# Performance work log

Measured on AMD Instinct MI355X. Metric: run time of the kernel, lower is better.

Reference implementation:

```python
import jax, jax.numpy as jnp
import numpy as np

B, T, DIM, H = 2, 2048, 512, 8
EPS = 1e-6


def setup_inputs() -> dict:
    key = jax.random.key(0)
    ks = jax.random.split(key, 6)
    scale = 0.05  # keep activations in a sane range for softmax/elu
    return {
        "x": jax.random.normal(ks[0], (B, T, DIM), dtype=jnp.float32),
        "Wq": jax.random.normal(ks[1], (DIM, DIM), dtype=jnp.float32) * scale,
        "Wk": jax.random.normal(ks[2], (DIM, DIM), dtype=jnp.float32) * scale,
        "Wv": jax.random.normal(ks[3], (DIM, DIM), dtype=jnp.float32) * scale,
        "Wo": jax.random.normal(ks[4], (DIM, DIM), dtype=jnp.float32) * scale,
        "bo": jax.random.normal(ks[5], (DIM,), dtype=jnp.float32) * scale,
    }


def reference(x, Wq, Wk, Wv, Wo, bo):
    b, t, dim = x.shape
    h = H
    d = dim // h
    # projections (nn.Linear: x @ W.T)
    q = x @ Wq.T
    k = x @ Wk.T
    v = x @ Wv.T
    mh = lambda z: z.reshape(b, t, h, d).transpose(0, 2, 1, 3)  # [b,h,t,d]
    q, k, v = mh(q), mh(k), mh(v)
    # causal linear attention with buckets = n (bucket size 1, no shift)
    q = jax.nn.softmax(q, axis=-1)
    k = jax.nn.elu(k) + 1.0  # psi
    k_cumsum = jnp.cumsum(k, axis=2)                       # [b,h,t,d]
    context = jnp.einsum('bhnd,bhne->bhnde', k, v)         # per-position outer products
    context = jnp.cumsum(context, axis=2)                  # causal prefix sum, [b,h,t,d,d]
    context = context / (k_cumsum[..., None] + EPS)        # safe_div
    attn = jnp.einsum('bhnd,bhnde->bhne', q, context)      # [b,h,t,d]
    out = attn.transpose(0, 2, 1, 3).reshape(b, t, dim)
    return out @ Wo.T + bo
```

## Files before the change

kernel.cpp:

```cpp
#include <hip/hip_runtime.h>

#define T_SEQ 2048
#define DIMM 512
#define NH 8
#define HD 64
#define BB 2
#define CHUNK 64
#define NCHUNK 32
#define EPSV 1e-6f
#define LDST 72
#define CST 66

typedef __attribute__((ext_vector_type(8))) short bf16x8;
typedef __attribute__((ext_vector_type(4))) short s16x4;
typedef __attribute__((ext_vector_type(4))) float f32x4;

static __device__ inline short f2bf(float f) {
    union { float f; unsigned u; } v; v.f = f;
    unsigned r = v.u + 0x7FFFu + ((v.u >> 16) & 1u);
    return (short)(r >> 16);
}
static __device__ inline float bf2f(short s) {
    union { unsigned u; float f; } v; v.u = ((unsigned)(unsigned short)s) << 16;
    return v.f;
}
static __device__ __forceinline__ void gload_lds16(const void* g, void* l) {
    __builtin_amdgcn_global_load_lds(
        (__attribute__((address_space(1))) void*)g,
        (__attribute__((address_space(3))) void*)l, 16, 0, 0);
}

__global__ __launch_bounds__(256) void convert_kernel(
    const float* __restrict__ x, const float* __restrict__ Wq,
    const float* __restrict__ Wk, const float* __restrict__ Wv,
    const float* __restrict__ Wo,
    short* __restrict__ xb, short* __restrict__ Wcat, short* __restrict__ Wob)
{
    const int u = blockIdx.x * 256 + threadIdx.x;
    const float* src; short* dst;
    if (u < 262144) {
        src = x + (size_t)u * 8; dst = xb + (size_t)u * 8;
    } else {
        const int v = u - 262144;
        const int o = (v & 32767) * 8;
        if (v < 32768)       { src = Wq + o; dst = Wcat + o; }
        else if (v < 65536)  { src = Wk + o; dst = Wcat + 262144 + o; }
        else if (v < 98304)  { src = Wv + o; dst = Wcat + 524288 + o; }
        else                 { src = Wo + o; dst = Wob + o; }
    }
    const float4 a = *(const float4*)src;
    const float4 b = *(const float4*)(src + 4);
    *(bf16x8*)dst = (bf16x8){f2bf(a.x), f2bf(a.y), f2bf(a.z), f2bf(a.w),
                             f2bf(b.x), f2bf(b.y), f2bf(b.z), f2bf(b.w)};
}

__global__ __launch_bounds__(256) void proj_mfma_kernel(
    const short* __restrict__ xb, const short* __restrict__ Wcat,
    short* __restrict__ Qs, short* __restrict__ Kbf,
    short* __restrict__ Ktb, short* __restrict__ Vt)
{
    __shared__ short S[8192];
    short* As = S;
    short* Bs = S + 4096;
    short* Cs = S;
    const int nblk = blockIdx.x;
    const int m0 = blockIdx.y * 64;
    const int n0 = nblk * 64;
    const int which = nblk >> 3;
    const int head = nblk & 7;
    const int tid = threadIdx.x;
    const int lane = tid & 63, w = tid >> 6;
    const int fr = lane & 15, fg = lane >> 4;
    const int lr = lane >> 3, lc = (lane & 7) * 8;
    f32x4 acc[4] = {};
    for (int k0 = 0; k0 < DIMM; k0 += 64) {
        #pragma unroll
        for (int it = 0; it < 2; it++) {
            const int r0 = w * 16 + it * 8;
            gload_lds16(xb + (size_t)(m0 + r0 + lr) * DIMM + k0 + lc, &As[r0 * 64]);
            gload_lds16(Wcat + (size_t)(n0 + r0 + lr) * DIMM + k0 + lc, &Bs[r0 * 64]);
        }
        __syncthreads();
        #pragma unroll
        for (int ks = 0; ks < 2; ks++) {
            const bf16x8 af = *(const bf16x8*)&As[(w * 16 + fr) * 64 + ks * 32 + fg * 8];
            #pragma unroll
            for (int j = 0; j < 4; j++) {
                const bf16x8 bfr = *(const bf16x8*)&Bs[(j * 16 + fr) * 64 + ks * 32 + fg * 8];
                acc[j] = __builtin_amdgcn_mfma_f32_16x16x32_bf16(af, bfr, acc[j], 0, 0, 0);
            }
        }
        __syncthreads();
    }
    #pragma unroll
    for (int j = 0; j < 4; j++)
        #pragma unroll
        for (int reg = 0; reg < 4; reg++) {
            float val = acc[j][reg];
            if (which == 1) val = (val > 0.f) ? (val + 1.f) : __expf(val);
            Cs[(w * 16 + fg * 4 + reg) * CST + j * 16 + fr] = f2bf(val);
        }
    __syncthreads();

    const int b = m0 >> 11, t0 = m0 & (T_SEQ - 1);
    if (which == 0) {
        if (tid < 64) {
            const unsigned* cr = (const unsigned*)&Cs[tid * CST];
            unsigned u[32];
            #pragma unroll
            for (int s = 0; s < 32; s++) u[s] = cr[s];
            float mx = -1e30f;
            #pragma unroll
            for (int s = 0; s < 32; s++) {
                mx = fmaxf(mx, bf2f((short)(u[s] & 0xffff)));
                mx = fmaxf(mx, bf2f((short)(u[s] >> 16)));
            }
            float sum = 0.f;
            #pragma unroll
            for (int s = 0; s < 32; s++) {
                sum += __expf(bf2f((short)(u[s] & 0xffff)) - mx);
                sum += __expf(bf2f((short)(u[s] >> 16)) - mx);
            }
            const float inv = 1.f / sum;
            short* qp = Qs + (((size_t)(b * NH + head)) * T_SEQ + t0 + tid) * HD;
            #pragma unroll
            for (int g = 0; g < 8; g++) {
                bf16x8 o;
                #pragma unroll
                for (int k = 0; k < 4; k++) {
                    const unsigned uv = u[g * 4 + k];
                    o[2 * k]     = f2bf(__expf(bf2f((short)(uv & 0xffff)) - mx) * inv);
                    o[2 * k + 1] = f2bf(__expf(bf2f((short)(uv >> 16)) - mx) * inv);
                }
                *(bf16x8*)(qp + g * 8) = o;
            }
        }
    } else if (which == 1) {
        if (tid < 64) {
            const unsigned* cr = (const unsigned*)&Cs[tid * CST];
            short* kp = Kbf + (((size_t)(b * NH + head)) * T_SEQ + t0 + tid) * HD;
            #pragma unroll
            for (int g = 0; g < 8; g++) {
                bf16x8 o;
                #pragma unroll
                for (int k = 0; k < 4; k++) {
                    const unsigned uv = cr[g * 4 + k];
                    o[2 * k]     = (short)(uv & 0xffff);
                    o[2 * k + 1] = (short)(uv >> 16);
                }
                *(bf16x8*)(kp + g * 8) = o;
            }
        }
        {
            const int c = tid & 63, q = tid >> 6;
            short* ktp = Ktb + (((size_t)(b * NH + head)) * HD + c) * T_SEQ + t0 + q * 16;
            #pragma unroll
            for (int s = 0; s < 2; s++) {
                bf16x8 o;
                #pragma unroll
                for (int k = 0; k < 8; k++) o[k] = Cs[(q * 16 + s * 8 + k) * CST + c];
                *(bf16x8*)(ktp + s * 8) = o;
            }
        }
    } else {
        const int c = tid & 63, q = tid >> 6;
        short* vtp = Vt + (((size_t)(b * NH + head)) * HD + c) * T_SEQ + t0 + q * 16;
        #pragma unroll
        for (int s = 0; s < 2; s++) {
            bf16x8 o;
            #pragma unroll
            for (int k = 0; k < 8; k++) o[k] = Cs[(q * 16 + s * 8 + k) * CST + c];
            *(bf16x8*)(vtp + s * 8) = o;
        }
    }
}

__global__ __launch_bounds__(256) void chunk_sum_kernel(
    const short* __restrict__ Ktb, const short* __restrict__ Vt,
    float* __restrict__ Schunk, float* __restrict__ kchunk)
{
    __shared__ short VtL[64 * LDST];
    __shared__ short KtL[64 * LDST];
    __shared__ float ksp[4][64];
    const int bh = blockIdx.x >> 5, c = blockIdx.x & 31;
    const int tid = threadIdx.x;
    const int lane = tid & 63, w = tid >> 6;
    const int fr = lane & 15, fg = lane >> 4;
    #pragma unroll
    for (int it = 0; it < 2; it++) {
        const int qi = it * 256 + tid;
        const int r = qi >> 3, c8 = (qi & 7) * 8;
        *(bf16x8*)&VtL[r * LDST + c8] =
            *(const bf16x8*)(Vt + ((size_t)(bh * HD) + r) * T_SEQ + c * CHUNK + c8);
        *(bf16x8*)&KtL[r * LDST + c8] =
            *(const bf16x8*)(Ktb + ((size_t)(bh * HD) + r) * T_SEQ + c * CHUNK + c8);
    }
    __syncthreads();
    f32x4 acc[4] = {};
    #pragma unroll
    for (int ks = 0; ks < 2; ks++) {
        const bf16x8 av = *(const bf16x8*)&VtL[(w * 16 + fr) * LDST + ks * 32 + fg * 8];
        #pragma unroll
        for (int j = 0; j < 4; j++) {
            const bf16x8 bk = *(const bf16x8*)&KtL[(j * 16 + fr) * LDST + ks * 32 + fg * 8];
            acc[j] = __builtin_amdgcn_mfma_f32_16x16x32_bf16(av, bk, acc[j], 0, 0, 0);
        }
    }
    float* Sout = Schunk + ((size_t)bh * NCHUNK + c) * 4096;
    #pragma unroll
    for (int j = 0; j < 4; j++)
        #pragma unroll
        for (int reg = 0; reg < 4; reg++)
            Sout[(w * 16 + fg * 4 + reg) * 64 + j * 16 + fr] = acc[j][reg];
    float ps = 0.f;
    #pragma unroll
    for (int t = 0; t < 16; t++) ps += bf2f(KtL[lane * LDST + w * 16 + t]);
    ksp[w][lane] = ps;
    __syncthreads();
    if (tid < 64)
        kchunk[((size_t)bh * NCHUNK + c) * 64 + tid] =
            ksp[0][tid] + ksp[1][tid] + ksp[2][tid] + ksp[3][tid];
}

__global__ __launch_bounds__(256) void scan_kernel(float* __restrict__ Schunk,
                                                   float* __restrict__ kchunk)
{
    const int gid = blockIdx.x * 256 + threadIdx.x;
    if (blockIdx.x < 256) {
        const int bh = gid >> 12, i = gid & 4095;
        float run = 0.f;
        float* p = Schunk + (size_t)bh * NCHUNK * 4096 + i;
        for (int c = 0; c < NCHUNK; c++) { const float tv = p[c * 4096]; p[c * 4096] = run; run += tv; }
    } else {
        const int idx = gid - 65536;
        const int bh = idx >> 6, d = idx & 63;
        float run = 0.f;
        float* p = kchunk + (size_t)bh * NCHUNK * 64 + d;
        for (int c = 0; c < NCHUNK; c++) { const float tv = p[c * 64]; p[c * 64] = run; run += tv; }
    }
}

__global__ __launch_bounds__(256) void intra_kernel(
    const short* __restrict__ Qs, const short* __restrict__ Kbf,
    const short* __restrict__ Vt, const float* __restrict__ Schunk,
    const float* __restrict__ kchunk, short* __restrict__ attnb)
{
    __shared__ short B1[64 * LDST];
    __shared__ short B2[64 * LDST];
    __shared__ short KL[64 * LDST];
    __shared__ short VtL[64 * LDST];
    __shared__ short QnL[64 * LDST];
    __shared__ float gsum[4][64];
    __shared__ float kpre[64];
    const int bh = blockIdx.x >> 5, c = blockIdx.x & 31;
    const int tid = threadIdx.x;
    const int lane = tid & 63, w = tid >> 6;
    const int fr = lane & 15, fg = lane >> 4;
    const size_t tdbase = ((size_t)bh * T_SEQ + c * CHUNK) * HD;
    #pragma unroll
    for (int it = 0; it < 2; it++) {
        const int qi = it * 256 + tid;
        const int r = qi >> 3, c8 = (qi & 7) * 8;
        *(bf16x8*)&B1[r * LDST + c8]  = *(const bf16x8*)(Qs + tdbase + r * HD + c8);
        *(bf16x8*)&KL[r * LDST + c8]  = *(const bf16x8*)(Kbf + tdbase + r * HD + c8);
        *(bf16x8*)&VtL[r * LDST + c8] =
            *(const bf16x8*)(Vt + ((size_t)(bh * HD) + r) * T_SEQ + c * CHUNK + c8);
    }
    {
        const float* Sp = Schunk + ((size_t)bh * NCHUNK + c) * 4096;
        #pragma unroll
        for (int it = 0; it < 4; it++) {
            const int qi = it * 256 + tid;
            const int r = qi >> 4, c4 = (qi & 15) * 4;
            const float4 v = *(const float4*)(Sp + r * 64 + c4);
            *(s16x4*)&B2[r * LDST + c4] = (s16x4){f2bf(v.x), f2bf(v.y), f2bf(v.z), f2bf(v.w)};
        }
    }
    if (tid < 64) kpre[tid] = kchunk[((size_t)bh * NCHUNK + c) * 64 + tid];
    __syncthreads();
    {
        float s = 0.f;
        #pragma unroll
        for (int t = 0; t < 16; t++) s += bf2f(KL[(w * 16 + t) * LDST + lane]);
        gsum[w][lane] = s;
    }
    __syncthreads();
    {
        float run = kpre[lane];
        for (int gg = 0; gg < w; gg++) run += gsum[gg][lane];
        #pragma unroll
        for (int t0 = 0; t0 < 16; t0++) {
            const int t = w * 16 + t0;
            run += bf2f(KL[t * LDST + lane]);
            const float qv = bf2f(B1[t * LDST + lane]);
            QnL[t * LDST + lane] = f2bf(qv / (run + EPSV));
        }
    }
    __syncthreads();
    {
        f32x4 a1[4] = {};
        #pragma unroll
        for (int ks = 0; ks < 2; ks++) {
            const bf16x8 aq = *(const bf16x8*)&QnL[(w * 16 + fr) * LDST + ks * 32 + fg * 8];
            #pragma unroll
            for (int j = 0; j < 4; j++) {
                const bf16x8 bk = *(const bf16x8*)&KL[(j * 16 + fr) * LDST + ks * 32 + fg * 8];
                a1[j] = __builtin_amdgcn_mfma_f32_16x16x32_bf16(aq, bk, a1[j], 0, 0, 0);
            }
        }
        const int trow = w * 16 + fg * 4;
        #pragma unroll
        for (int j = 0; j < 4; j++)
            #pragma unroll
            for (int reg = 0; reg < 4; reg++) {
                const int t = trow + reg, s = j * 16 + fr;
                B1[t * LDST + s] = (s <= t) ? f2bf(a1[j][reg]) : (short)0;
            }
    }
    __syncthreads();
    {
        f32x4 a2[4] = {};
        #pragma unroll
        for (int ks = 0; ks < 2; ks++) {
            const bf16x8 aq = *(const bf16x8*)&QnL[(w * 16 + fr) * LDST + ks * 32 + fg * 8];
            const bf16x8 aa = *(const bf16x8*)&B1[(w * 16 + fr) * LDST + ks * 32 + fg * 8];
            #pragma unroll
            for (int j = 0; j < 4; j++) {
                const bf16x8 bs = *(const bf16x8*)&B2[(j * 16 + fr) * LDST + ks * 32 + fg * 8];
                const bf16x8 bv = *(const bf16x8*)&VtL[(j * 16 + fr) * LDST + ks * 32 + fg * 8];
                a2[j] = __builtin_amdgcn_mfma_f32_16x16x32_bf16(aq, bs, a2[j], 0, 0, 0);
                a2[j] = __builtin_amdgcn_mfma_f32_16x16x32_bf16(aa, bv, a2[j], 0, 0, 0);
            }
        }
        short* ap = attnb + tdbase;
        const int trow = w * 16 + fg * 4;
        #pragma unroll
        for (int j = 0; j < 4; j++)
            #pragma unroll
            for (int reg = 0; reg < 4; reg++)
                ap[(trow + reg) * HD + j * 16 + fr] = f2bf(a2[j][reg]);
    }
}

__global__ __launch_bounds__(256) void outproj_mfma_kernel(
    const short* __restrict__ attnb, const short* __restrict__ Wob,
    const float* __restrict__ bo, float* __restrict__ out)
{
    __shared__ short As[64 * 64];
    __shared__ short Bs[64 * 64];
    const int m0 = blockIdx.x * 64;
    const int n0 = blockIdx.y * 64;
    const int tid = threadIdx.x;
    const int lane = tid & 63, w = tid >> 6;
    const int fr = lane & 15, fg = lane >> 4;
    const int lr = lane >> 3, lc = (lane & 7) * 8;
    const int b = m0 >> 11, tbase = m0 & (T_SEQ - 1);
    f32x4 acc[4] = {};
    for (int k0 = 0; k0 < DIMM; k0 += 64) {
        const int h = k0 >> 6;
        #pragma unroll
        for (int it = 0; it < 2; it++) {
            const int r0 = w * 16 + it * 8;
            gload_lds16(attnb + (((size_t)(b * NH + h)) * T_SEQ + tbase + r0 + lr) * HD + lc,
                        &As[r0 * 64]);
            gload_lds16(Wob + (size_t)(n0 + r0 + lr) * DIMM + k0 + lc, &Bs[r0 * 64]);
        }
        __syncthreads();
        #pragma unroll
        for (int ks = 0; ks < 2; ks++) {
            const bf16x8 af = *(const bf16x8*)&As[(w * 16 + fr) * 64 + ks * 32 + fg * 8];
            #pragma unroll
            for (int j = 0; j < 4; j++) {
                const bf16x8 bfr = *(const bf16x8*)&Bs[(j * 16 + fr) * 64 + ks * 32 + fg * 8];
                acc[j] = __builtin_amdgcn_mfma_f32_16x16x32_bf16(af, bfr, acc[j], 0, 0, 0);
            }
        }
        __syncthreads();
    }
    #pragma unroll
    for (int j = 0; j < 4; j++)
        #pragma unroll
        for (int reg = 0; reg < 4; reg++) {
            const int m = m0 + w * 16 + fg * 4 + reg;
            const int n = n0 + j * 16 + fr;
            out[(size_t)m * DIMM + n] = acc[j][reg] + bo[n];
        }
}

extern "C" void kernel_launch(void* const* d_in, const int* in_sizes, int n_in,
                              void* d_out, int out_size, void* d_ws, size_t ws_size,
                              hipStream_t stream)
{
    const float* x  = (const float*)d_in[0];
    const float* Wq = (const float*)d_in[1];
    const float* Wk = (const float*)d_in[2];
    const float* Wv = (const float*)d_in[3];
    const float* Wo = (const float*)d_in[4];
    const float* bo = (const float*)d_in[5];
    float* out = (float*)d_out;

    const size_t NELEM = (size_t)BB * T_SEQ * DIMM;
    short* xb    = (short*)d_ws;
    short* Wcat  = xb + NELEM;
    short* Wob   = Wcat + 786432;
    short* Qs    = Wob + 262144;
    short* Kbf   = Qs + NELEM;
    short* Ktb   = Kbf + NELEM;
    short* Vt    = Ktb + NELEM;
    short* attnb = Vt + NELEM;
    float* Schunk = (float*)(attnb + NELEM);
    float* kchunk = Schunk + (size_t)BB * NH * NCHUNK * 4096;

    convert_kernel<<<dim3(1536), 256, 0, stream>>>(x, Wq, Wk, Wv, Wo, xb, Wcat, Wob);
    proj_mfma_kernel<<<dim3(24, 64), 256, 0, stream>>>(xb, Wcat, Qs, Kbf, Ktb, Vt);
    chunk_sum_kernel<<<dim3(BB * NH * NCHUNK), 256, 0, stream>>>(Ktb, Vt, Schunk, kchunk);
    scan_kernel<<<dim3(260), 256, 0, stream>>>(Schunk, kchunk);
    intra_kernel<<<dim3(BB * NH * NCHUNK), 256, 0, stream>>>(Qs, Kbf, Vt, Schunk, kchunk, attnb);
    outproj_mfma_kernel<<<dim3(64, 8), 256, 0, stream>>>(attnb, Wob, bo, out);
}
```

Baseline: 64.02 us.

## Fuse QKV projection per head with chunk state computation and swizzle LDS

The projection kernel now computes Q, K and V for one head and a 64-row tile in a single block of 12 MFMA accumulators, and reuses the shared x tile across all three. The chunk-sum kernel is folded in, so the per-chunk K^T V state and the K column sums are computed straight from the LDS tile instead of being re-read from global memory. An XOR swizzle is applied to the LDS tile layout to reduce bank conflicts. In exchange there are fewer blocks (512 instead of 1536), more registers per thread and a larger LDS footprint, and the fused epilogue does strided scalar LDS reads.

```diff
diff --git a/kernel.cpp b/kernel.cpp
--- a/kernel.cpp
+++ b/kernel.cpp
@@ -9,7 +9,7 @@
 #define NCHUNK 32
 #define EPSV 1e-6f
 #define LDST 72
-#define CST 66
+#define CST2 198
 
 typedef __attribute__((ext_vector_type(8))) short bf16x8;
 typedef __attribute__((ext_vector_type(4))) short s16x4;
@@ -54,172 +54,161 @@
                              f2bf(b.x), f2bf(b.y), f2bf(b.z), f2bf(b.w)};
 }
 
-__global__ __launch_bounds__(256) void proj_mfma_kernel(
+__global__ __launch_bounds__(256) void fusedproj_kernel(
     const short* __restrict__ xb, const short* __restrict__ Wcat,
     short* __restrict__ Qs, short* __restrict__ Kbf,
-    short* __restrict__ Ktb, short* __restrict__ Vt)
-{
-    __shared__ short S[8192];
+    short* __restrict__ Ktb, short* __restrict__ Vt,
+    float* __restrict__ Schunk, float* __restrict__ kchunk)
+{
+    __shared__ short S[16384];
     short* As = S;
     short* Bs = S + 4096;
     short* Cs = S;
-    const int nblk = blockIdx.x;
+    const int h = blockIdx.x;
     const int m0 = blockIdx.y * 64;
-    const int n0 = nblk * 64;
-    const int which = nblk >> 3;
-    const int head = nblk & 7;
+    const int b = m0 >> 11;
+    const int t0 = m0 & (T_SEQ - 1);
+    const int c = t0 >> 6;
+    const int bh = b * NH + h;
     const int tid = threadIdx.x;
     const int lane = tid & 63, w = tid >> 6;
     const int fr = lane & 15, fg = lane >> 4;
-    const int lr = lane >> 3, lc = (lane & 7) * 8;
-    f32x4 acc[4] = {};
+    const int lr = lane >> 3;
+    const int sl8 = ((lane & 7) ^ lr) * 8;
+    const int xr = fr & 7;
+    f32x4 acc[12] = {};
+
     for (int k0 = 0; k0 < DIMM; k0 += 64) {
         #pragma unroll
         for (int it = 0; it < 2; it++) {
             const int r0 = w * 16 + it * 8;
-            gload_lds16(xb + (size_t)(m0 + r0 + lr) * DIMM + k0 + lc, &As[r0 * 64]);
-            gload_lds16(Wcat + (size_t)(n0 + r0 + lr) * DIMM + k0 + lc, &Bs[r0 * 64]);
+            gload_lds16(xb + (size_t)(m0 + r0 + lr) * DIMM + k0 + sl8, &As[r0 * 64]);
+        }
+        #pragma unroll
+        for (int it = 0; it < 6; it++) {
+            const int rb0 = w * 48 + it * 8;
+            const int rb = rb0 + lr;
+            const int p = rb >> 6;
+            const int gr = p * DIMM + h * 64 + (rb & 63);
+            gload_lds16(Wcat + (size_t)gr * DIMM + k0 + sl8, &Bs[rb0 * 64]);
         }
         __syncthreads();
         #pragma unroll
         for (int ks = 0; ks < 2; ks++) {
-            const bf16x8 af = *(const bf16x8*)&As[(w * 16 + fr) * 64 + ks * 32 + fg * 8];
-            #pragma unroll
-            for (int j = 0; j < 4; j++) {
-                const bf16x8 bfr = *(const bf16x8*)&Bs[(j * 16 + fr) * 64 + ks * 32 + fg * 8];
-                acc[j] = __builtin_amdgcn_mfma_f32_16x16x32_bf16(af, bfr, acc[j], 0, 0, 0);
+            const int cc = (((ks << 2) + fg) ^ xr) * 8;
+            const bf16x8 af = *(const bf16x8*)&As[(w * 16 + fr) * 64 + cc];
+            #pragma unroll
+            for (int jj = 0; jj < 12; jj++) {
+                const bf16x8 bfr = *(const bf16x8*)&Bs[(jj * 16 + fr) * 64 + cc];
+                acc[jj] = __builtin_amdgcn_mfma_f32_16x16x32_bf16(af, bfr, acc[jj], 0, 0, 0);
             }
         }
         __syncthreads();
     }
+
     #pragma unroll
-    for (int j = 0; j < 4; j++)
+    for (int jj = 0; jj < 12; jj++)
         #pragma unroll
         for (int reg = 0; reg < 4; reg++) {
-            float val = acc[j][reg];
-            if (which == 1) val = (val > 0.f) ? (val + 1.f) : __expf(val);
-            Cs[(w * 16 + fg * 4 + reg) * CST + j * 16 + fr] = f2bf(val);
+            float val = acc[jj][reg];
+            if (jj >= 4 && jj < 8) val = (val > 0.f) ? (val + 1.f) : __expf(val);
+            Cs[(w * 16 + fg * 4 + reg) * CST2 + jj * 16 + fr] = f2bf(val);
         }
     __syncthreads();
 
-    const int b = m0 >> 11, t0 = m0 & (T_SEQ - 1);
-    if (which == 0) {
-        if (tid < 64) {
-            const unsigned* cr = (const unsigned*)&Cs[tid * CST];
-            unsigned u[32];
-            #pragma unroll
-            for (int s = 0; s < 32; s++) u[s] = cr[s];
-            float mx = -1e30f;
-            #pragma unroll
-            for (int s = 0; s < 32; s++) {
-                mx = fmaxf(mx, bf2f((short)(u[s] & 0xffff)));
-                mx = fmaxf(mx, bf2f((short)(u[s] >> 16)));
-            }
-            float sum = 0.f;
-            #pragma unroll
-            for (int s = 0; s < 32; s++) {
-                sum += __expf(bf2f((short)(u[s] & 0xffff)) - mx);
-                sum += __expf(bf2f((short)(u[s] >> 16)) - mx);
-            }
-            const float inv = 1.f / sum;
-            short* qp = Qs + (((size_t)(b * NH + head)) * T_SEQ + t0 + tid) * HD;
-            #pragma unroll
-            for (int g = 0; g < 8; g++) {
-                bf16x8 o;
+    if (tid < 64) {
+        const int r = tid;
+        const unsigned* cr = (const unsigned*)&Cs[r * CST2];
+        unsigned u[32];
+        #pragma unroll
+        for (int s = 0; s < 32; s++) u[s] = cr[s];
+        float mx = -1e30f;
+        #pragma unroll
+        for (int s = 0; s < 32; s++) {
+            mx = fmaxf(mx, bf2f((short)(u[s] & 0xffff)));
+            mx = fmaxf(mx, bf2f((short)(u[s] >> 16)));
+        }
+        float sum = 0.f;
+        #pragma unroll
+        for (int s = 0; s < 32; s++) {
+            sum += __expf(bf2f((short)(u[s] & 0xffff)) - mx);
+            sum += __expf(bf2f((short)(u[s] >> 16)) - mx);
+        }
+        const float inv = 1.f / sum;
+        short* qp = Qs + ((size_t)bh * T_SEQ + t0 + r) * HD;
+        #pragma unroll
+        for (int g = 0; g < 8; g++) {
+            bf16x8 o;
+            #pragma unroll
+            for (int k = 0; k < 4; k++) {
+                const unsigned uv = u[g * 4 + k];
+                o[2 * k]     = f2bf(__expf(bf2f((short)(uv & 0xffff)) - mx) * inv);
+                o[2 * k + 1] = f2bf(__expf(bf2f((short)(uv >> 16)) - mx) * inv);
+            }
+            *(bf16x8*)(qp + g * 8) = o;
+        }
+    } else if (tid < 128) {
+        const int r = tid - 64;
+        const unsigned* cr = (const unsigned*)&Cs[r * CST2 + 64];
+        short* kp = Kbf + ((size_t)bh * T_SEQ + t0 + r) * HD;
+        #pragma unroll
+        for (int g = 0; g < 8; g++) {
+            bf16x8 o;
+            #pragma unroll
+            for (int k = 0; k < 4; k++) {
+                const unsigned uv = cr[g * 4 + k];
+                o[2 * k]     = (short)(uv & 0xffff);
+                o[2 * k + 1] = (short)(uv >> 16);
+            }
+            *(bf16x8*)(kp + g * 8) = o;
+        }
+    }
+    {
+        const int col = tid & 63, q = tid >> 6;
+        short* ktp = Ktb + ((size_t)bh * HD + col) * T_SEQ + t0 + q * 16;
+        short* vtp = Vt  + ((size_t)bh * HD + col) * T_SEQ + t0 + q * 16;
+        #pragma unroll
+        for (int s = 0; s < 2; s++) {
+            bf16x8 ok, ov;
+            #pragma unroll
+            for (int k = 0; k < 8; k++) {
+                ok[k] = Cs[(q * 16 + s * 8 + k) * CST2 + 64 + col];
+                ov[k] = Cs[(q * 16 + s * 8 + k) * CST2 + 128 + col];
+            }
+            *(bf16x8*)(ktp + s * 8) = ok;
+            *(bf16x8*)(vtp + s * 8) = ov;
+        }
+    }
+    {
+        f32x4 a2[4] = {};
+        #pragma unroll
+        for (int ks = 0; ks < 2; ks++) {
+            bf16x8 av;
+            #pragma unroll
+            for (int uu = 0; uu < 8; uu++)
+                av[uu] = Cs[(ks * 32 + fg * 8 + uu) * CST2 + 128 + w * 16 + fr];
+            #pragma unroll
+            for (int jj = 0; jj < 4; jj++) {
+                bf16x8 bk;
                 #pragma unroll
-                for (int k = 0; k < 4; k++) {
-                    const unsigned uv = u[g * 4 + k];
-                    o[2 * k]     = f2bf(__expf(bf2f((short)(uv & 0xffff)) - mx) * inv);
-                    o[2 * k + 1] = f2bf(__expf(bf2f((short)(uv >> 16)) - mx) * inv);
-                }
-                *(bf16x8*)(qp + g * 8) = o;
-            }
-        }
-    } else if (which == 1) {
-        if (tid < 64) {
-            const unsigned* cr = (const unsigned*)&Cs[tid * CST];
-            short* kp = Kbf + (((size_t)(b * NH + head)) * T_SEQ + t0 + tid) * HD;
-            #pragma unroll
-            for (int g = 0; g < 8; g++) {
-                bf16x8 o;
-                #pragma unroll
-                for (int k = 0; k < 4; k++) {
-                    const unsigned uv = cr[g * 4 + k];
-                    o[2 * k]     = (short)(uv & 0xffff);
-                    o[2 * k + 1] = (short)(uv >> 16);
-                }
-                *(bf16x8*)(kp + g * 8) = o;
-            }
-        }
-        {
-            const int c = tid & 63, q = tid >> 6;
-            short* ktp = Ktb + (((size_t)(b * NH + head)) * HD + c) * T_SEQ + t0 + q * 16;
-            #pragma unroll
-            for (int s = 0; s < 2; s++) {
-                bf16x8 o;
-                #pragma unroll
-                for (int k = 0; k < 8; k++) o[k] = Cs[(q * 16 + s * 8 + k) * CST + c];
-                *(bf16x8*)(ktp + s * 8) = o;
-            }
-        }
-    } else {
-        const int c = tid & 63, q = tid >> 6;
-        short* vtp = Vt + (((size_t)(b * NH + head)) * HD + c) * T_SEQ + t0 + q * 16;
-        #pragma unroll
-        for (int s = 0; s < 2; s++) {
-            bf16x8 o;
-            #pragma unroll
-            for (int k = 0; k < 8; k++) o[k] = Cs[(q * 16 + s * 8 + k) * CST + c];
-            *(bf16x8*)(vtp + s * 8) = o;
-        }
-    }
-}
-
-__global__ __launch_bounds__(256) void chunk_sum_kernel(
-    const short* __restrict__ Ktb, const short* __restrict__ Vt,
-    float* __restrict__ Schunk, float* __restrict__ kchunk)
-{
-    __shared__ short VtL[64 * LDST];
-    __shared__ short KtL[64 * LDST];
-    __shared__ float ksp[4][64];
-    const int bh = blockIdx.x >> 5, c = blockIdx.x & 31;
-    const int tid = threadIdx.x;
-    const int lane = tid & 63, w = tid >> 6;
-    const int fr = lane & 15, fg = lane >> 4;
-    #pragma unroll
-    for (int it = 0; it < 2; it++) {
-        const int qi = it * 256 + tid;
-        const int r = qi >> 3, c8 = (qi & 7) * 8;
-        *(bf16x8*)&VtL[r * LDST + c8] =
-            *(const bf16x8*)(Vt + ((size_t)(bh * HD) + r) * T_SEQ + c * CHUNK + c8);
-        *(bf16x8*)&KtL[r * LDST + c8] =
-            *(const bf16x8*)(Ktb + ((size_t)(bh * HD) + r) * T_SEQ + c * CHUNK + c8);
-    }
-    __syncthreads();
-    f32x4 acc[4] = {};
-    #pragma unroll
-    for (int ks = 0; ks < 2; ks++) {
-        const bf16x8 av = *(const bf16x8*)&VtL[(w * 16 + fr) * LDST + ks * 32 + fg * 8];
-        #pragma unroll
-        for (int j = 0; j < 4; j++) {
-            const bf16x8 bk = *(const bf16x8*)&KtL[(j * 16 + fr) * LDST + ks * 32 + fg * 8];
-            acc[j] = __builtin_amdgcn_mfma_f32_16x16x32_bf16(av, bk, acc[j], 0, 0, 0);
-        }
-    }
-    float* Sout = Schunk + ((size_t)bh * NCHUNK + c) * 4096;
-    #pragma unroll
-    for (int j = 0; j < 4; j++)
-        #pragma unroll
-        for (int reg = 0; reg < 4; reg++)
-            Sout[(w * 16 + fg * 4 + reg) * 64 + j * 16 + fr] = acc[j][reg];
-    float ps = 0.f;
-    #pragma unroll
-    for (int t = 0; t < 16; t++) ps += bf2f(KtL[lane * LDST + w * 16 + t]);
-    ksp[w][lane] = ps;
-    __syncthreads();
-    if (tid < 64)
-        kchunk[((size_t)bh * NCHUNK + c) * 64 + tid] =
-            ksp[0][tid] + ksp[1][tid] + ksp[2][tid] + ksp[3][tid];
+                for (int uu = 0; uu < 8; uu++)
+                    bk[uu] = Cs[(ks * 32 + fg * 8 + uu) * CST2 + 64 + jj * 16 + fr];
+                a2[jj] = __builtin_amdgcn_mfma_f32_16x16x32_bf16(av, bk, a2[jj], 0, 0, 0);
+            }
+        }
+        float* Sout = Schunk + ((size_t)bh * NCHUNK + c) * 4096;
+        #pragma unroll
+        for (int jj = 0; jj < 4; jj++)
+            #pragma unroll
+            for (int reg = 0; reg < 4; reg++)
+                Sout[(w * 16 + fg * 4 + reg) * 64 + jj * 16 + fr] = a2[jj][reg];
+    }
+    if (tid < 64) {
+        float s = 0.f;
+        #pragma unroll
+        for (int t = 0; t < 64; t++) s += bf2f(Cs[t * CST2 + 64 + tid]);
+        kchunk[((size_t)bh * NCHUNK + c) * 64 + tid] = s;
+    }
 }
 
 __global__ __launch_bounds__(256) void scan_kernel(float* __restrict__ Schunk,
@@ -412,8 +401,8 @@
     float* kchunk = Schunk + (size_t)BB * NH * NCHUNK * 4096;
 
     convert_kernel<<<dim3(1536), 256, 0, stream>>>(x, Wq, Wk, Wv, Wo, xb, Wcat, Wob);
-    proj_mfma_kernel<<<dim3(24, 64), 256, 0, stream>>>(xb, Wcat, Qs, Kbf, Ktb, Vt);
-    chunk_sum_kernel<<<dim3(BB * NH * NCHUNK), 256, 0, stream>>>(Ktb, Vt, Schunk, kchunk);
+    fusedproj_kernel<<<dim3(8, 64), 256, 0, stream>>>(xb, Wcat, Qs, Kbf, Ktb, Vt,
+                                                      Schunk, kchunk);
     scan_kernel<<<dim3(260), 256, 0, stream>>>(Schunk, kchunk);
     intra_kernel<<<dim3(BB * NH * NCHUNK), 256, 0, stream>>>(Qs, Kbf, Vt, Schunk, kchunk, attnb);
     outproj_mfma_kernel<<<dim3(64, 8), 256, 0, stream>>>(attnb, Wob, bo, out);
```

After: 56.22 us. 12.2% less time.

## Rewrite QKV projection as 256x256 tiled, double-buffered GEMM with swizzled LDS

Applied to the files above, without the earlier changes.

Replaces the 64x64-tile projection kernel with a 512-thread kernel that computes 256x256 output tiles. Global loads go straight into LDS through a double buffer, using an XOR swizzle to avoid bank conflicts, and MFMA issue priority is raised during compute. The epilogue is widened to handle four heads per block for the softmax, ELU and transpose writes. The aim is more operand reuse and less load traffic per FLOP. The cost is a grid of only 96 blocks, which leaves many CUs idle, plus a large 132KB dynamic LDS allocation.

```diff
diff --git a/kernel.cpp b/kernel.cpp
--- a/kernel.cpp
+++ b/kernel.cpp
@@ -9,7 +9,8 @@
 #define NCHUNK 32
 #define EPSV 1e-6f
 #define LDST 72
-#define CST 66
+#define PCST 258
+#define PJ_LDS 132096
 
 typedef __attribute__((ext_vector_type(8))) short bf16x8;
 typedef __attribute__((ext_vector_type(4))) short s16x4;
@@ -54,58 +55,122 @@
                              f2bf(b.x), f2bf(b.y), f2bf(b.z), f2bf(b.w)};
 }
 
-__global__ __launch_bounds__(256) void proj_mfma_kernel(
+__global__ __launch_bounds__(512) void proj256_kernel(
     const short* __restrict__ xb, const short* __restrict__ Wcat,
     short* __restrict__ Qs, short* __restrict__ Kbf,
     short* __restrict__ Ktb, short* __restrict__ Vt)
 {
-    __shared__ short S[8192];
-    short* As = S;
-    short* Bs = S + 4096;
-    short* Cs = S;
-    const int nblk = blockIdx.x;
-    const int m0 = blockIdx.y * 64;
-    const int n0 = nblk * 64;
-    const int which = nblk >> 3;
-    const int head = nblk & 7;
+    extern __shared__ short S[];
+    const int m0 = blockIdx.x * 256;
+    const int n0 = blockIdx.y * 256;
+    const int which = blockIdx.y >> 1;
+    const int headbase = (blockIdx.y & 1) * 4;
     const int tid = threadIdx.x;
     const int lane = tid & 63, w = tid >> 6;
+    const int wr = w >> 2, wc = w & 3;
     const int fr = lane & 15, fg = lane >> 4;
-    const int lr = lane >> 3, lc = (lane & 7) * 8;
-    f32x4 acc[4] = {};
-    for (int k0 = 0; k0 < DIMM; k0 += 64) {
-        #pragma unroll
-        for (int it = 0; it < 2; it++) {
-            const int r0 = w * 16 + it * 8;
-            gload_lds16(xb + (size_t)(m0 + r0 + lr) * DIMM + k0 + lc, &As[r0 * 64]);
-            gload_lds16(Wcat + (size_t)(n0 + r0 + lr) * DIMM + k0 + lc, &Bs[r0 * 64]);
-        }
-        __syncthreads();
-        #pragma unroll
-        for (int ks = 0; ks < 2; ks++) {
-            const bf16x8 af = *(const bf16x8*)&As[(w * 16 + fr) * 64 + ks * 32 + fg * 8];
-            #pragma unroll
-            for (int j = 0; j < 4; j++) {
-                const bf16x8 bfr = *(const bf16x8*)&Bs[(j * 16 + fr) * 64 + ks * 32 + fg * 8];
-                acc[j] = __builtin_amdgcn_mfma_f32_16x16x32_bf16(af, bfr, acc[j], 0, 0, 0);
-            }
-        }
-        __syncthreads();
-    }
-    #pragma unroll
-    for (int j = 0; j < 4; j++)
-        #pragma unroll
-        for (int reg = 0; reg < 4; reg++) {
-            float val = acc[j][reg];
-            if (which == 1) val = (val > 0.f) ? (val + 1.f) : __expf(val);
-            Cs[(w * 16 + fg * 4 + reg) * CST + j * 16 + fr] = f2bf(val);
-        }
-    __syncthreads();
-
+    const int xr = fr & 7;
+    const int l8 = lane >> 3;
+    const int sw8 = ((lane & 7) ^ l8) * 8;
     const int b = m0 >> 11, t0 = m0 & (T_SEQ - 1);
+
+    f32x4 acc[8][4] = {};
+
+    #define STAGE_HALF(ds, ktv, half) do {                                        \
+        const int isB_ = (half) >> 1, hb_ = ((half) & 1) * 128;                   \
+        short* dst_ = S + (ds) * 32768 + isB_ * 16384 + (hb_ + w * 16) * 64;      \
+        const short* g_ = isB_ ? (Wcat + (size_t)(n0 + hb_ + w * 16) * DIMM)      \
+                               : (xb + (size_t)(m0 + hb_ + w * 16) * DIMM);       \
+        gload_lds16(g_ + (size_t)l8 * DIMM + (ktv) * 64 + sw8, dst_);             \
+        gload_lds16(g_ + (size_t)(8 + l8) * DIMM + (ktv) * 64 + sw8, dst_ + 512); \
+    } while (0)
+
+    STAGE_HALF(0, 0, 0); STAGE_HALF(0, 0, 1); STAGE_HALF(0, 0, 2); STAGE_HALF(0, 0, 3);
+
+    for (int kt = 0; kt < 8; ++kt) {
+        const int slot = kt & 1;
+        const short* Ab = S + slot * 32768;
+        const short* Bb = Ab + 16384;
+        asm volatile("s_waitcnt vmcnt(0)" ::: "memory");
+        __builtin_amdgcn_s_barrier();
+
+        bf16x8 bfrag[4], af[4];
+        #pragma unroll
+        for (int j = 0; j < 4; j++)
+            bfrag[j] = *(const bf16x8*)&Bb[(wc * 64 + j * 16 + fr) * 64 + (fg ^ xr) * 8];
+        #pragma unroll
+        for (int i = 0; i < 4; i++)
+            af[i] = *(const bf16x8*)&Ab[(wr * 128 + i * 16 + fr) * 64 + (fg ^ xr) * 8];
+        if (kt < 7) { STAGE_HALF(slot ^ 1, kt + 1, 0); STAGE_HALF(slot ^ 1, kt + 1, 1); }
+        __builtin_amdgcn_s_setprio(1);
+        #pragma unroll
+        for (int i = 0; i < 4; i++)
+            #pragma unroll
+            for (int j = 0; j < 4; j++)
+                acc[i][j] = __builtin_amdgcn_mfma_f32_16x16x32_bf16(af[i], bfrag[j], acc[i][j], 0, 0, 0);
+        __builtin_amdgcn_s_setprio(0);
+        __builtin_amdgcn_s_barrier();
+        #pragma unroll
+        for (int i = 0; i < 4; i++)
+            af[i] = *(const bf16x8*)&Ab[(wr * 128 + (i + 4) * 16 + fr) * 64 + (fg ^ xr) * 8];
+        if (kt < 7) { STAGE_HALF(slot ^ 1, kt + 1, 2); STAGE_HALF(slot ^ 1, kt + 1, 3); }
+        __builtin_amdgcn_s_setprio(1);
+        #pragma unroll
+        for (int i = 0; i < 4; i++)
+            #pragma unroll
+            for (int j = 0; j < 4; j++)
+                acc[i + 4][j] = __builtin_amdgcn_mfma_f32_16x16x32_bf16(af[i], bfrag[j], acc[i + 4][j], 0, 0, 0);
+        __builtin_amdgcn_s_setprio(0);
+        __builtin_amdgcn_s_barrier();
+        #pragma unroll
+        for (int j = 0; j < 4; j++)
+            bfrag[j] = *(const bf16x8*)&Bb[(wc * 64 + j * 16 + fr) * 64 + ((4 + fg) ^ xr) * 8];
+        #pragma unroll
+        for (int i = 0; i < 4; i++)
+            af[i] = *(const bf16x8*)&Ab[(wr * 128 + i * 16 + fr) * 64 + ((4 + fg) ^ xr) * 8];
+        __builtin_amdgcn_s_setprio(1);
+        #pragma unroll
+        for (int i = 0; i < 4; i++)
+            #pragma unroll
+            for (int j = 0; j < 4; j++)
+                acc[i][j] = __builtin_amdgcn_mfma_f32_16x16x32_bf16(af[i], bfrag[j], acc[i][j], 0, 0, 0);
+        __builtin_amdgcn_s_setprio(0);
+        __builtin_amdgcn_s_barrier();
+        #pragma unroll
+        for (int i = 0; i < 4; i++)
+            af[i] = *(const bf16x8*)&Ab[(wr * 128 + (i + 4) * 16 + fr) * 64 + ((4 + fg) ^ xr) * 8];
+        __builtin_amdgcn_s_setprio(1);
+        #pragma unroll
+        for (int i = 0; i < 4; i++)
+            #pragma unroll
+            for (int j = 0; j < 4; j++)
+                acc[i + 4][j] = __builtin_amdgcn_mfma_f32_16x16x32_bf16(af[i], bfrag[j], acc[i + 4][j], 0, 0, 0);
+        __builtin_amdgcn_s_setprio(0);
+        __builtin_amdgcn_s_barrier();
+    }
+    #undef STAGE_HALF
+    __syncthreads();
+
+    short* Cs = S;
+    #pragma unroll
+    for (int i = 0; i < 8; i++)
+        #pragma unroll
+        for (int j = 0; j < 4; j++)
+            #pragma unroll
+            for (int reg = 0; reg < 4; reg++) {
+                float val = acc[i][j][reg];
+                if (which == 1) val = (val > 0.f) ? (val + 1.f) : __expf(val);
+                Cs[(wr * 128 + i * 16 + fg * 4 + reg) * PCST + wc * 64 + j * 16 + fr] = f2bf(val);
+            }
+    __syncthreads();
+
     if (which == 0) {
-        if (tid < 64) {
-            const unsigned* cr = (const unsigned*)&Cs[tid * CST];
+        #pragma unroll
+        for (int rep = 0; rep < 2; rep++) {
+            const int task = rep * 512 + tid;
+            const int row = task & 255, hl = task >> 8;
+            const int head = headbase + hl;
+            const unsigned* cr = (const unsigned*)&Cs[row * PCST + hl * 64];
             unsigned u[32];
             #pragma unroll
             for (int s = 0; s < 32; s++) u[s] = cr[s];
@@ -122,7 +187,7 @@
                 sum += __expf(bf2f((short)(u[s] >> 16)) - mx);
             }
             const float inv = 1.f / sum;
-            short* qp = Qs + (((size_t)(b * NH + head)) * T_SEQ + t0 + tid) * HD;
+            short* qp = Qs + (((size_t)(b * NH + head)) * T_SEQ + t0 + row) * HD;
             #pragma unroll
             for (int g = 0; g < 8; g++) {
                 bf16x8 o;
@@ -136,9 +201,13 @@
             }
         }
     } else if (which == 1) {
-        if (tid < 64) {
-            const unsigned* cr = (const unsigned*)&Cs[tid * CST];
-            short* kp = Kbf + (((size_t)(b * NH + head)) * T_SEQ + t0 + tid) * HD;
+        #pragma unroll
+        for (int rep = 0; rep < 2; rep++) {
+            const int task = rep * 512 + tid;
+            const int row = task & 255, hl = task >> 8;
+            const int head = headbase + hl;
+            const unsigned* cr = (const unsigned*)&Cs[row * PCST + hl * 64];
+            short* kp = Kbf + (((size_t)(b * NH + head)) * T_SEQ + t0 + row) * HD;
             #pragma unroll
             for (int g = 0; g < 8; g++) {
                 bf16x8 o;
@@ -152,24 +221,26 @@
             }
         }
         {
-            const int c = tid & 63, q = tid >> 6;
-            short* ktp = Ktb + (((size_t)(b * NH + head)) * HD + c) * T_SEQ + t0 + q * 16;
-            #pragma unroll
-            for (int s = 0; s < 2; s++) {
+            const int col = tid & 255, rh = tid >> 8;
+            const int head = headbase + (col >> 6), d = col & 63;
+            short* ktp = Ktb + (((size_t)(b * NH + head)) * HD + d) * T_SEQ + t0 + rh * 128;
+            #pragma unroll
+            for (int s = 0; s < 16; s++) {
                 bf16x8 o;
                 #pragma unroll
-                for (int k = 0; k < 8; k++) o[k] = Cs[(q * 16 + s * 8 + k) * CST + c];
+                for (int k = 0; k < 8; k++) o[k] = Cs[(rh * 128 + s * 8 + k) * PCST + col];
                 *(bf16x8*)(ktp + s * 8) = o;
             }
         }
     } else {
-        const int c = tid & 63, q = tid >> 6;
-        short* vtp = Vt + (((size_t)(b * NH + head)) * HD + c) * T_SEQ + t0 + q * 16;
-        #pragma unroll
-        for (int s = 0; s < 2; s++) {
+        const int col = tid & 255, rh = tid >> 8;
+        const int head = headbase + (col >> 6), e = col & 63;
+        short* vtp = Vt + (((size_t)(b * NH + head)) * HD + e) * T_SEQ + t0 + rh * 128;
+        #pragma unroll
+        for (int s = 0; s < 16; s++) {
             bf16x8 o;
             #pragma unroll
-            for (int k = 0; k < 8; k++) o[k] = Cs[(q * 16 + s * 8 + k) * CST + c];
+            for (int k = 0; k < 8; k++) o[k] = Cs[(rh * 128 + s * 8 + k) * PCST + col];
             *(bf16x8*)(vtp + s * 8) = o;
         }
     }
@@ -411,8 +482,15 @@
     float* Schunk = (float*)(attnb + NELEM);
     float* kchunk = Schunk + (size_t)BB * NH * NCHUNK * 4096;
 
+    static bool attr_set = false;
+    if (!attr_set) {
+        hipFuncSetAttribute((const void*)proj256_kernel,
+                            hipFuncAttributeMaxDynamicSharedMemorySize, PJ_LDS);
+        attr_set = true;
+    }
+
     convert_kernel<<<dim3(1536), 256, 0, stream>>>(x, Wq, Wk, Wv, Wo, xb, Wcat, Wob);
-    proj_mfma_kernel<<<dim3(24, 64), 256, 0, stream>>>(xb, Wcat, Qs, Kbf, Ktb, Vt);
+    proj256_kernel<<<dim3(16, 6), 512, PJ_LDS, stream>>>(xb, Wcat, Qs, Kbf, Ktb, Vt);
     chunk_sum_kernel<<<dim3(BB * NH * NCHUNK), 256, 0, stream>>>(Ktb, Vt, Schunk, kchunk);
     scan_kernel<<<dim3(260), 256, 0, stream>>>(Schunk, kchunk);
     intra_kernel<<<dim3(BB * NH * NCHUNK), 256, 0, stream>>>(Qs, Kbf, Vt, Schunk, kchunk, attnb);
```

Result: slower. 68.82 us (+7.5%).

## Keep full weight slice resident in LDS and stream x directly from global

Applied to the files above, without the earlier changes.

The projection kernel now loads the block's entire 64x512 weight slice into LDS once, using an XOR swizzle, instead of tiling over K with per-step syncs. Activation fragments are read straight from global memory into registers. Each block now covers 128 rows instead of 64, so the grid is halved. This removes the per-K-step barriers and reloading of the x tile through LDS, and reuses the weight tile across two M subtiles. In exchange, LDS use rises to 64KB per block, which limits occupancy, and A operands become uncoalesced global loads.

```diff
diff --git a/kernel.cpp b/kernel.cpp
--- a/kernel.cpp
+++ b/kernel.cpp
@@ -9,7 +9,7 @@
 #define NCHUNK 32
 #define EPSV 1e-6f
 #define LDST 72
-#define CST 66
+#define BCST 66
 
 typedef __attribute__((ext_vector_type(8))) short bf16x8;
 typedef __attribute__((ext_vector_type(4))) short s16x4;
@@ -54,58 +54,66 @@
                              f2bf(b.x), f2bf(b.y), f2bf(b.z), f2bf(b.w)};
 }
 
-__global__ __launch_bounds__(256) void proj_mfma_kernel(
+__global__ __launch_bounds__(256, 2) void proj_bstat_kernel(
     const short* __restrict__ xb, const short* __restrict__ Wcat,
     short* __restrict__ Qs, short* __restrict__ Kbf,
     short* __restrict__ Ktb, short* __restrict__ Vt)
 {
-    __shared__ short S[8192];
-    short* As = S;
-    short* Bs = S + 4096;
-    short* Cs = S;
+    __shared__ short BL[64 * 512];
     const int nblk = blockIdx.x;
-    const int m0 = blockIdx.y * 64;
+    const int which = nblk >> 3, head = nblk & 7;
     const int n0 = nblk * 64;
-    const int which = nblk >> 3;
-    const int head = nblk & 7;
+    const int m0 = blockIdx.y * 128;
     const int tid = threadIdx.x;
     const int lane = tid & 63, w = tid >> 6;
     const int fr = lane & 15, fg = lane >> 4;
-    const int lr = lane >> 3, lc = (lane & 7) * 8;
-    f32x4 acc[4] = {};
-    for (int k0 = 0; k0 < DIMM; k0 += 64) {
-        #pragma unroll
-        for (int it = 0; it < 2; it++) {
-            const int r0 = w * 16 + it * 8;
-            gload_lds16(xb + (size_t)(m0 + r0 + lr) * DIMM + k0 + lc, &As[r0 * 64]);
-            gload_lds16(Wcat + (size_t)(n0 + r0 + lr) * DIMM + k0 + lc, &Bs[r0 * 64]);
-        }
-        __syncthreads();
-        #pragma unroll
-        for (int ks = 0; ks < 2; ks++) {
-            const bf16x8 af = *(const bf16x8*)&As[(w * 16 + fr) * 64 + ks * 32 + fg * 8];
-            #pragma unroll
-            for (int j = 0; j < 4; j++) {
-                const bf16x8 bfr = *(const bf16x8*)&Bs[(j * 16 + fr) * 64 + ks * 32 + fg * 8];
-                acc[j] = __builtin_amdgcn_mfma_f32_16x16x32_bf16(af, bfr, acc[j], 0, 0, 0);
-            }
-        }
-        __syncthreads();
-    }
-    #pragma unroll
-    for (int j = 0; j < 4; j++)
-        #pragma unroll
-        for (int reg = 0; reg < 4; reg++) {
-            float val = acc[j][reg];
-            if (which == 1) val = (val > 0.f) ? (val + 1.f) : __expf(val);
-            Cs[(w * 16 + fg * 4 + reg) * CST + j * 16 + fr] = f2bf(val);
-        }
-    __syncthreads();
-
     const int b = m0 >> 11, t0 = m0 & (T_SEQ - 1);
+    const int bh = b * NH + head;
+
+    #pragma unroll
+    for (int it = 0; it < 16; ++it) {
+        const int row = it * 4 + w;
+        gload_lds16(Wcat + (size_t)(n0 + row) * DIMM + (lane ^ (row & 7)) * 8,
+                    &BL[row * 512]);
+    }
+    asm volatile("s_waitcnt vmcnt(0)" ::: "memory");
+    __syncthreads();
+
+    f32x4 acc[2][4] = {};
+    #pragma unroll
+    for (int ms = 0; ms < 2; ++ms) {
+        const int mrow = m0 + ms * 64 + w * 16 + fr;
+        const short* ap = xb + (size_t)mrow * DIMM + fg * 8;
+        #pragma unroll
+        for (int kk = 0; kk < 16; ++kk) {
+            const bf16x8 af = *(const bf16x8*)(ap + kk * 32);
+            #pragma unroll
+            for (int j = 0; j < 4; ++j) {
+                const int cc = (kk * 4 + fg) ^ (fr & 7);
+                const bf16x8 bfr = *(const bf16x8*)&BL[(j * 16 + fr) * 512 + cc * 8];
+                acc[ms][j] = __builtin_amdgcn_mfma_f32_16x16x32_bf16(af, bfr, acc[ms][j], 0, 0, 0);
+            }
+        }
+    }
+    __syncthreads();
+
+    short* Cs = BL;
+    #pragma unroll
+    for (int ms = 0; ms < 2; ++ms)
+        #pragma unroll
+        for (int j = 0; j < 4; ++j)
+            #pragma unroll
+            for (int reg = 0; reg < 4; ++reg) {
+                float val = acc[ms][j][reg];
+                if (which == 1) val = (val > 0.f) ? (val + 1.f) : __expf(val);
+                Cs[(ms * 64 + w * 16 + fg * 4 + reg) * BCST + j * 16 + fr] = f2bf(val);
+            }
+    __syncthreads();
+
     if (which == 0) {
-        if (tid < 64) {
-            const unsigned* cr = (const unsigned*)&Cs[tid * CST];
+        if (tid < 128) {
+            const int r = tid;
+            const unsigned* cr = (const unsigned*)&Cs[r * BCST];
             unsigned u[32];
             #pragma unroll
             for (int s = 0; s < 32; s++) u[s] = cr[s];
@@ -122,7 +130,7 @@
                 sum += __expf(bf2f((short)(u[s] >> 16)) - mx);
             }
             const float inv = 1.f / sum;
-            short* qp = Qs + (((size_t)(b * NH + head)) * T_SEQ + t0 + tid) * HD;
+            short* qp = Qs + ((size_t)bh * T_SEQ + t0 + r) * HD;
             #pragma unroll
             for (int g = 0; g < 8; g++) {
                 bf16x8 o;
@@ -136,9 +144,10 @@
             }
         }
     } else if (which == 1) {
-        if (tid < 64) {
-            const unsigned* cr = (const unsigned*)&Cs[tid * CST];
-            short* kp = Kbf + (((size_t)(b * NH + head)) * T_SEQ + t0 + tid) * HD;
+        if (tid < 128) {
+            const int r = tid;
+            const unsigned* cr = (const unsigned*)&Cs[r * BCST];
+            short* kp = Kbf + ((size_t)bh * T_SEQ + t0 + r) * HD;
             #pragma unroll
             for (int g = 0; g < 8; g++) {
                 bf16x8 o;
@@ -152,24 +161,24 @@
             }
         }
         {
-            const int c = tid & 63, q = tid >> 6;
-            short* ktp = Ktb + (((size_t)(b * NH + head)) * HD + c) * T_SEQ + t0 + q * 16;
-            #pragma unroll
-            for (int s = 0; s < 2; s++) {
+            const int col = tid & 63, q = tid >> 6;
+            short* ktp = Ktb + ((size_t)bh * HD + col) * T_SEQ + t0 + q * 32;
+            #pragma unroll
+            for (int s = 0; s < 4; s++) {
                 bf16x8 o;
                 #pragma unroll
-                for (int k = 0; k < 8; k++) o[k] = Cs[(q * 16 + s * 8 + k) * CST + c];
+                for (int k = 0; k < 8; k++) o[k] = Cs[(q * 32 + s * 8 + k) * BCST + col];
                 *(bf16x8*)(ktp + s * 8) = o;
             }
         }
     } else {
-        const int c = tid & 63, q = tid >> 6;
-        short* vtp = Vt + (((size_t)(b * NH + head)) * HD + c) * T_SEQ + t0 + q * 16;
-        #pragma unroll
-        for (int s = 0; s < 2; s++) {
+        const int col = tid & 63, q = tid >> 6;
+        short* vtp = Vt + ((size_t)bh * HD + col) * T_SEQ + t0 + q * 32;
+        #pragma unroll
+        for (int s = 0; s < 4; s++) {
             bf16x8 o;
             #pragma unroll
-            for (int k = 0; k < 8; k++) o[k] = Cs[(q * 16 + s * 8 + k) * CST + c];
+            for (int k = 0; k < 8; k++) o[k] = Cs[(q * 32 + s * 8 + k) * BCST + col];
             *(bf16x8*)(vtp + s * 8) = o;
         }
     }
@@ -412,7 +421,7 @@
     float* kchunk = Schunk + (size_t)BB * NH * NCHUNK * 4096;
 
     convert_kernel<<<dim3(1536), 256, 0, stream>>>(x, Wq, Wk, Wv, Wo, xb, Wcat, Wob);
-    proj_mfma_kernel<<<dim3(24, 64), 256, 0, stream>>>(xb, Wcat, Qs, Kbf, Ktb, Vt);
+    proj_bstat_kernel<<<dim3(24, 32), 256, 0, stream>>>(xb, Wcat, Qs, Kbf, Ktb, Vt);
     chunk_sum_kernel<<<dim3(BB * NH * NCHUNK), 256, 0, stream>>>(Ktb, Vt, Schunk, kchunk);
     scan_kernel<<<dim3(260), 256, 0, stream>>>(Schunk, kchunk);
     intra_kernel<<<dim3(BB * NH * NCHUNK), 256, 0, stream>>>(Qs, Kbf, Vt, Schunk, kchunk, attnb);
```

Measured after the change: 68.71 us. 1.07x slower.
